# Performance work log

Hardware: AMD Instinct MI355X
Metric: run time of the kernel (lower is better)

Reference implementation:

```python
import jax, jax.numpy as jnp
import numpy as np

B = 8192
D_S, D_W, D_P, D_E, D_C, D_Z = 1024, 1024, 512, 1024, 512, 512
H_P = 2 * D_P          # particle hidden_dim default
RANK = D_W // 4        # low-rank A factor
EPS = 1e-5             # torch LayerNorm default eps


def _ln(x, g, b):
    m = jnp.mean(x, axis=-1, keepdims=True)
    v = jnp.var(x, axis=-1, keepdims=True)
    return (x - m) * jax.lax.rsqrt(v + EPS) * g + b


def setup_inputs() -> dict:
    key = jax.random.key(0)
    ks = iter(jax.random.split(key, 48))
    def randn(shape, scale=1.0):
        return jax.random.normal(next(ks), shape, dtype=jnp.float32) * scale
    def lin(dout, din):  # torch Linear: W [out,in], b [out]
        s = 1.0 / np.sqrt(din)
        return randn((dout, din), s), randn((dout,), s)
    inp = {}
    inp["s_prev"] = randn((B, D_S))
    inp["w_prev"] = randn((B, D_W))
    inp["p_prev"] = randn((B, D_P))
    inp["e_t"] = randn((B, D_E))
    inp["c_t"] = randn((B, D_C))
    d_in = D_S + D_E + D_C
    # fusion_net: Linear -> LN -> ReLU -> Linear
    inp["fw1"], inp["fb1"] = lin(2 * D_Z, d_in)
    inp["fln_g"] = jnp.ones((2 * D_Z,), jnp.float32)
    inp["fln_b"] = jnp.zeros((2 * D_Z,), jnp.float32)
    inp["fw2"], inp["fb2"] = lin(D_Z, 2 * D_Z)
    # wave subsystem
    inp["A_diag"] = jnp.zeros((D_W,), jnp.float32)
    inp["A_U"] = randn((D_W, RANK), 0.01)
    inp["A_V"] = randn((D_W, RANK), 0.01)
    inp["amod_w"], inp["amod_b"] = lin(D_W, D_C)
    inp["bnet_w"], inp["bnet_b"] = lin(D_W, D_C + D_Z)
    # particle subsystem phi
    inp["pw1"], inp["pb1"] = lin(H_P, D_P + D_Z + D_C)
    inp["pln_g"] = jnp.ones((H_P,), jnp.float32)
    inp["pln_b"] = jnp.zeros((H_P,), jnp.float32)
    inp["pw2"], inp["pb2"] = lin(H_P // 2, H_P)
    inp["pw3"], inp["pb3"] = lin(D_P, H_P // 2)
    # gate + mixing projections + output norm
    inp["gw"], inp["gb"] = lin(D_S, d_in)
    inp["uw"] = randn((D_S, D_W), 1.0 / np.sqrt(D_W))
    inp["up"] = randn((D_S, D_P), 1.0 / np.sqrt(D_P))
    inp["oln_g"] = jnp.ones((D_S,), jnp.float32)
    inp["oln_b"] = jnp.zeros((D_S,), jnp.float32)
    return inp


def reference(s_prev, w_prev, p_prev, e_t, c_t,
              fw1, fb1, fln_g, fln_b, fw2, fb2,
              A_diag, A_U, A_V, amod_w, amod_b, bnet_w, bnet_b,
              pw1, pb1, pln_g, pln_b, pw2, pb2, pw3, pb3,
              gw, gb, uw, up, oln_g, oln_b):
    # fusion: z_t = Linear(ReLU(LN(Linear([s||e||c]))))
    fin = jnp.concatenate([s_prev, e_t, c_t], axis=-1)      # [B, d_s+d_e+d_c]
    h = jax.nn.relu(_ln(fin @ fw1.T + fb1, fln_g, fln_b))
    z_t = h @ fw2.T + fb2                                   # [B, d_z]
    # wave: A = (diag(tanh(A_diag)*0.9) + A_U A_V^T) * mod[None,:]
    # so (A w)[b,i] = sum_j A_base[i,j] * (mod*w)[b,j] -> (mod*w) @ A_base^T
    A_base = jnp.diag(jnp.tanh(A_diag) * 0.9) + A_U @ A_V.T  # [d_w, d_w]
    mod = jnp.tanh(c_t @ amod_w.T + amod_b)                  # [B, d_w]
    w_linear = (mod * w_prev) @ A_base.T
    b_in = jnp.concatenate([c_t, z_t], axis=-1)
    w_t = w_linear + b_in @ bnet_w.T + bnet_b                # [B, d_w]
    # particle: p_t = p_prev + tanh(MLP([p||z||c]))
    pin = jnp.concatenate([p_prev, z_t, c_t], axis=-1)
    h1 = jax.nn.relu(_ln(pin @ pw1.T + pb1, pln_g, pln_b))
    h2 = jax.nn.relu(h1 @ pw2.T + pb2)
    p_t = p_prev + jnp.tanh(h2 @ pw3.T + pb3)                # [B, d_p]
    # gated mixing
    g_t = jax.nn.sigmoid(fin @ gw.T + gb)                    # [B, d_s]
    s_t = s_prev + g_t * (p_t @ up.T) + (1.0 - g_t) * (w_t @ uw.T)
    s_t = _ln(s_t, oln_g, oln_b)
    return (s_t, w_t, p_t)
```

## Files before the change

kernel.cpp:

```cpp
#include <hip/hip_runtime.h>
#include <math.h>

typedef unsigned short u16;
typedef __attribute__((ext_vector_type(8))) short short8;
typedef __attribute__((ext_vector_type(4))) float f32x4;

#define AS1C(p) ((const __attribute__((address_space(1))) void*)(p))
#define AS3(p)  ((__attribute__((address_space(3))) void*)(p))

static __device__ __forceinline__ float b2f(u16 h) {
    union { unsigned u; float f; } c; c.u = ((unsigned)h) << 16; return c.f;
}
static __device__ __forceinline__ u16 f2b(float f) {
    union { float f; unsigned u; } c; c.f = f;
    unsigned r = c.u + 0x7FFFu + ((c.u >> 16) & 1u);
    return (u16)(r >> 16);
}

#define EP_NONE     0
#define EP_RELU     1
#define EP_SIGMOID  2
#define EP_TANH_MUL 3
#define EP_TANH_ADD 4
#define EP_DIAG     5

struct GDesc {
    const u16* A;
    const u16* W;
    const float* bias;
    const float* auxf;
    u16* outb;
    float* outf;
    int lda, ldd, N, K, ep, nbm;
};

struct GArgs { GDesc d0, d1, d2; int s1, s2; };

__global__ __launch_bounds__(512, 2)
void gemm_v2(GArgs ga)
{
    __shared__ __align__(16) u16 LDS[65536];

    const int bid = (int)blockIdx.x;
    GDesc dd = (bid < ga.s1) ? ga.d0 : ((bid < ga.s2) ? ga.d1 : ga.d2);
    const int b = bid - ((bid < ga.s1) ? 0 : ((bid < ga.s2) ? ga.s1 : ga.s2));

    const int tid  = threadIdx.x;
    const int lane = tid & 63;
    const int wid  = tid >> 6;
    const int wr   = wid >> 2;
    const int wc   = wid & 3;

    const int bm = b % dd.nbm;
    const int bn = b / dd.nbm;
    const int lda = dd.lda, K = dd.K, N = dd.N, ldd = dd.ldd;
    const int nkt = K >> 6;

    const int srow  = tid >> 3;
    const int sslot = tid & 7;
    const int sgcol = (sslot ^ (srow & 7)) * 8;
    const u16* Ag = dd.A + (size_t)(bm * 256 + srow) * lda + sgcol;
    const u16* Wg = dd.W + (size_t)(bn * 256 + srow) * K + sgcol;
    const int ldst = tid * 8;

    f32x4 acc[8][4];
#pragma unroll
    for (int m = 0; m < 8; ++m)
#pragma unroll
        for (int n = 0; n < 4; ++n) acc[m][n] = (f32x4){0.f, 0.f, 0.f, 0.f};

    const int swz  = (lane & 7) << 4;
    const int cnat = (lane >> 4) << 4;
    const int aRow = (wr * 64 + (lane & 15)) * 64;
    const int bRow = (wc * 32 + (lane & 15)) * 64;
    const u16* pA00 = LDS + aRow + ((cnat ^ swz) >> 1);
    const u16* pA10 = LDS + aRow + ((((64) | cnat) ^ swz) >> 1);
    const u16* pA01 = pA00 + 32768;
    const u16* pA11 = pA10 + 32768;
    const u16* pB00 = LDS + 16384 + bRow + ((cnat ^ swz) >> 1);
    const u16* pB10 = LDS + 16384 + bRow + ((((64) | cnat) ^ swz) >> 1);
    const u16* pB01 = pB00 + 32768;
    const u16* pB11 = pB10 + 32768;

    short8 A0f[4][2], A1f[4][2], B0f[2][2], B1f[2][2];

#define READ_A(AF, PK0, PK1, MHOFF)                                              \
    {                                                                            \
        _Pragma("unroll")                                                        \
        for (int mm = 0; mm < 4; ++mm) {                                         \
            AF[mm][0] = *(const short8*)((PK0) + (MHOFF) + mm * 1024);           \
            AF[mm][1] = *(const short8*)((PK1) + (MHOFF) + mm * 1024);           \
        }                                                                        \
    }
#define READ_B(BF, PK0, PK1, NHOFF)                                              \
    {                                                                            \
        _Pragma("unroll")                                                        \
        for (int nn = 0; nn < 2; ++nn) {                                         \
            BF[nn][0] = *(const short8*)((PK0) + (NHOFF) + nn * 1024);           \
            BF[nn][1] = *(const short8*)((PK1) + (NHOFF) + nn * 1024);           \
        }                                                                        \
    }

#define STAGE_A(bufi, k0_, h)                                                    \
    {                                                                            \
        u16* d_ = &LDS[(bufi) * 32768 + ldst];                                   \
        _Pragma("unroll")                                                        \
        for (int j = 2 * (h); j < 2 * (h) + 2; ++j)                              \
            __builtin_amdgcn_global_load_lds(AS1C(Ag + (size_t)(j * 64) * lda + (k0_)), \
                                             AS3(d_ + j * 4096), 16, 0, 0);      \
    }
#define STAGE_B(bufi, k0_, h)                                                    \
    {                                                                            \
        u16* d_ = &LDS[(bufi) * 32768 + 16384 + ldst];                           \
        _Pragma("unroll")                                                        \
        for (int j = 2 * (h); j < 2 * (h) + 2; ++j)                              \
            __builtin_amdgcn_global_load_lds(AS1C(Wg + (size_t)(j * 64) * K + (k0_)),   \
                                             AS3(d_ + j * 4096), 16, 0, 0);      \
    }

#define VW4()                                                                    \
    {                                                                            \
        __builtin_amdgcn_sched_barrier(0);                                       \
        asm volatile("s_waitcnt vmcnt(4)" ::: "memory");                         \
        __builtin_amdgcn_sched_barrier(0);                                       \
        __builtin_amdgcn_s_barrier();                                            \
        __builtin_amdgcn_sched_barrier(0);                                       \
    }

#define QMFMA(AF, BF, mh, nh)                                                    \
    {                                                                            \
        __builtin_amdgcn_s_setprio(1);                                           \
        _Pragma("unroll")                                                        \
        for (int mm = 0; mm < 4; ++mm)                                           \
            _Pragma("unroll")                                                    \
            for (int nn = 0; nn < 2; ++nn)                                       \
                _Pragma("unroll")                                                \
                for (int ks = 0; ks < 2; ++ks)                                   \
                    acc[(mh) * 4 + mm][(nh) * 2 + nn] =                          \
                        __builtin_amdgcn_mfma_f32_16x16x32_bf16(                 \
                            AF[mm][ks], BF[nn][ks], acc[(mh) * 4 + mm][(nh) * 2 + nn], 0, 0, 0); \
        __builtin_amdgcn_s_setprio(0);                                           \
    }

#define TILE(NBUF, CA0, CA1, CBp0, CBp1, NA0, NA1, NBp0, NBp1, ktv)              \
    {                                                                            \
        const int ka_ = ((ktv) + 1 < nkt) ? (ktv) + 1 : nkt - 1;                 \
        const int k0n = ka_ << 6;                                                \
            \
        STAGE_A(NBUF, k0n, 0);                                                   \
        VW4();                                                                   \
        QMFMA(A0f, B0f, 0, 0);                                                   \
        READ_B(B1f, CBp0, CBp1, 8192);                                           \
            \
        STAGE_B(NBUF, k0n, 0);                                                   \
        VW4();                                                                   \
        QMFMA(A0f, B1f, 0, 1);                                                   \
        READ_A(A1f, CA0, CA1, 8192);                                             \
         \
        STAGE_B(NBUF, k0n, 1);                                                   \
        VW4();                                                                   \
        QMFMA(A1f, B1f, 1, 1);                                                   \
        READ_A(A0f, NA0, NA1, 0);                                                \
         \
        STAGE_A(NBUF, k0n, 1);                                                   \
        VW4();                                                                   \
        QMFMA(A1f, B0f, 1, 0);                                                   \
        READ_B(B0f, NBp0, NBp1, 0);                                              \
    }

    STAGE_A(0, 0, 0);
    __builtin_amdgcn_sched_barrier(0);
    STAGE_B(0, 0, 0);
    __builtin_amdgcn_sched_barrier(0);
    STAGE_B(0, 0, 1);
    __builtin_amdgcn_sched_barrier(0);
    STAGE_A(0, 0, 1);
    __builtin_amdgcn_sched_barrier(0);
    asm volatile("s_waitcnt vmcnt(4)" ::: "memory");
    __builtin_amdgcn_sched_barrier(0);
    __builtin_amdgcn_s_barrier();
    __builtin_amdgcn_sched_barrier(0);
    READ_A(A0f, pA00, pA10, 0);
    READ_B(B0f, pB00, pB10, 0);

    for (int kt = 0; kt < nkt; kt += 2) {
        TILE(1, pA00, pA10, pB00, pB10, pA01, pA11, pB01, pB11, kt);
        TILE(0, pA01, pA11, pB01, pB11, pA00, pA10, pB00, pB10, kt + 1);
    }

#undef READ_A
#undef READ_B
#undef STAGE_A
#undef STAGE_B
#undef VW4
#undef QMFMA
#undef TILE

    const int ep = dd.ep;
#pragma unroll
    for (int n = 0; n < 4; ++n) {
        const int C = bn * 256 + (n >> 1) * 128 + wc * 32 + (n & 1) * 16 + (lane & 15);
        const float bv = dd.bias ? dd.bias[C] : 0.f;
#pragma unroll
        for (int m = 0; m < 8; ++m) {
            const int R0 = bm * 256 + (m >> 2) * 128 + wr * 64 + (m & 3) * 16 + ((lane >> 4) << 2);
#pragma unroll
            for (int j = 0; j < 4; ++j) {
                const int R = R0 + j;
                float v = acc[m][n][j] + bv;
                if (ep == EP_RELU)          v = fmaxf(v, 0.f);
                else if (ep == EP_SIGMOID)  v = 1.f / (1.f + expf(-v));
                else if (ep == EP_TANH_MUL) v = tanhf(v) * dd.auxf[(size_t)R * N + C];
                else if (ep == EP_TANH_ADD) v = dd.auxf[(size_t)R * N + C] + tanhf(v);
                else if (ep == EP_DIAG)     { if (R == C) v += 0.9f * tanhf(dd.auxf[R]); }
                dd.outb[(size_t)R * ldd + C] = f2b(v);
                if (dd.outf) dd.outf[(size_t)R * N + C] = v;
            }
        }
    }
}

template<bool RELU>
__global__ __launch_bounds__(256)
void ln1024(u16* __restrict__ X, const float* __restrict__ gam, const float* __restrict__ bet)
{
    const int row = blockIdx.x;
    u16* xp = X + (size_t)row * 1024 + threadIdx.x * 4;
    u16 loc[4];
    *(uint2*)loc = *(const uint2*)xp;
    float x0 = b2f(loc[0]), x1 = b2f(loc[1]), x2 = b2f(loc[2]), x3 = b2f(loc[3]);
    float s = x0 + x1 + x2 + x3;
    float q = x0 * x0 + x1 * x1 + x2 * x2 + x3 * x3;
#pragma unroll
    for (int off = 32; off; off >>= 1) { s += __shfl_xor(s, off); q += __shfl_xor(q, off); }
    __shared__ float sm[8];
    const int wave = threadIdx.x >> 6, lane = threadIdx.x & 63;
    if (lane == 0) { sm[wave] = s; sm[4 + wave] = q; }
    __syncthreads();
    s = sm[0] + sm[1] + sm[2] + sm[3];
    q = sm[4] + sm[5] + sm[6] + sm[7];
    const float mean = s * (1.f / 1024.f);
    const float var  = q * (1.f / 1024.f) - mean * mean;
    const float inv  = rsqrtf(var + 1e-5f);
    const int cb = threadIdx.x * 4;
#pragma unroll
    for (int j = 0; j < 4; ++j) {
        float y = (b2f(loc[j]) - mean) * inv * gam[cb + j] + bet[cb + j];
        if (RELU) y = fmaxf(y, 0.f);
        loc[j] = f2b(y);
    }
    *(uint2*)xp = *(uint2*)loc;
}

__global__ __launch_bounds__(256)
void mix_ln(const float* __restrict__ sp, const u16* __restrict__ gt,
            const u16* __restrict__ pm, const u16* __restrict__ wm,
            const float* __restrict__ og, const float* __restrict__ ob,
            float* __restrict__ out)
{
    const int row = blockIdx.x;
    const size_t base = (size_t)row * 1024 + threadIdx.x * 4;
    float4 lsp = *(const float4*)(sp + base);
    u16 lg[4], lp[4], lw[4];
    *(uint2*)lg = *(const uint2*)(gt + base);
    *(uint2*)lp = *(const uint2*)(pm + base);
    *(uint2*)lw = *(const uint2*)(wm + base);
    float x[4];
    const float* lspp = (const float*)&lsp;
#pragma unroll
    for (int j = 0; j < 4; ++j) {
        float g = b2f(lg[j]);
        x[j] = lspp[j] + g * b2f(lp[j]) + (1.f - g) * b2f(lw[j]);
    }
    float s = x[0] + x[1] + x[2] + x[3];
    float q = x[0]*x[0] + x[1]*x[1] + x[2]*x[2] + x[3]*x[3];
#pragma unroll
    for (int off = 32; off; off >>= 1) { s += __shfl_xor(s, off); q += __shfl_xor(q, off); }
    __shared__ float sm[8];
    const int wave = threadIdx.x >> 6, lane = threadIdx.x & 63;
    if (lane == 0) { sm[wave] = s; sm[4 + wave] = q; }
    __syncthreads();
    s = sm[0] + sm[1] + sm[2] + sm[3];
    q = sm[4] + sm[5] + sm[6] + sm[7];
    const float mean = s * (1.f / 1024.f);
    const float var  = q * (1.f / 1024.f) - mean * mean;
    const float inv  = rsqrtf(var + 1e-5f);
    const int cb = threadIdx.x * 4;
    float4 o;
    float* op = (float*)&o;
#pragma unroll
    for (int j = 0; j < 4; ++j)
        op[j] = (x[j] - mean) * inv * og[cb + j] + ob[cb + j];
    *(float4*)(out + base) = o;
}

struct CDesc { const void* src; u16* dst; int srcCols8; int dstStride; int dstOff; unsigned end; int isbf16; };
struct CArgs { CDesc d[16]; unsigned total; };

__global__ __launch_bounds__(256)
void multi_copy(CArgs ca)
{
    const unsigned idx = blockIdx.x * 256 + threadIdx.x;
    if (idx >= ca.total) return;
    int i = 0; unsigned start = 0;
    while (idx >= ca.d[i].end) { start = ca.d[i].end; ++i; }
    const CDesc cd = ca.d[i];
    const unsigned local = idx - start;
    const int r = local / cd.srcCols8;
    const int c = local % cd.srcCols8;
    u16 o[8];
    if (cd.isbf16) {
        *(uint4*)o = *(const uint4*)((const u16*)cd.src + ((size_t)r * cd.srcCols8 + c) * 8);
    } else {
        const float* s = (const float*)cd.src + ((size_t)r * cd.srcCols8 + c) * 8;
        const float4 a = *(const float4*)s;
        const float4 bq = *(const float4*)(s + 4);
        const float* ap = (const float*)&a;
        const float* bp = (const float*)&bq;
#pragma unroll
        for (int j = 0; j < 4; ++j) { o[j] = f2b(ap[j]); o[4 + j] = f2b(bp[j]); }
    }
    *(uint4*)(cd.dst + (size_t)r * cd.dstStride + cd.dstOff + (size_t)c * 8) = *(uint4*)o;
}

extern "C" void kernel_launch(void* const* d_in, const int* in_sizes, int n_in,
                              void* d_out, int out_size, void* d_ws, size_t ws_size,
                              hipStream_t stream)
{
    const float* s_prev = (const float*)d_in[0];
    const float* w_prev = (const float*)d_in[1];
    const float* p_prev = (const float*)d_in[2];
    const float* e_t    = (const float*)d_in[3];
    const float* c_t    = (const float*)d_in[4];
    const float* fw1    = (const float*)d_in[5];
    const float* fb1    = (const float*)d_in[6];
    const float* fln_g  = (const float*)d_in[7];
    const float* fln_b  = (const float*)d_in[8];
    const float* fw2    = (const float*)d_in[9];
    const float* fb2    = (const float*)d_in[10];
    const float* A_diag = (const float*)d_in[11];
    const float* A_U    = (const float*)d_in[12];
    const float* A_V    = (const float*)d_in[13];
    const float* amod_w = (const float*)d_in[14];
    const float* amod_b = (const float*)d_in[15];
    const float* bnet_w = (const float*)d_in[16];
    const float* bnet_b = (const float*)d_in[17];
    const float* pw1    = (const float*)d_in[18];
    const float* pb1    = (const float*)d_in[19];
    const float* pln_g  = (const float*)d_in[20];
    const float* pln_b  = (const float*)d_in[21];
    const float* pw2    = (const float*)d_in[22];
    const float* pb2    = (const float*)d_in[23];
    const float* pw3    = (const float*)d_in[24];
    const float* pb3    = (const float*)d_in[25];
    const float* gw     = (const float*)d_in[26];
    const float* gb     = (const float*)d_in[27];
    const float* uw     = (const float*)d_in[28];
    const float* up     = (const float*)d_in[29];
    const float* oln_g  = (const float*)d_in[30];
    const float* oln_b  = (const float*)d_in[31];

    float* out_s = (float*)d_out;
    float* out_w = out_s + (size_t)8192 * 1024;
    float* out_p = out_w + (size_t)8192 * 1024;

    u16* ws = (u16*)d_ws;
    u16* FIN  = ws;
    u16* W_bf = ws + 12582912;
    u16* H    = ws + 20971520;
    u16* P_bf = H;
    u16* Z    = ws + 29360128;
    u16* G    = ws + 33554432;
    u16* ACAT = ws + 41943040;
    u16* PM   = ACAT;
    u16* WM   = ACAT + 8388608;
    u16* WCAT = ws + 58720256;
    u16* wb   = ws + 60817408;
    u16* fw1b  = wb;
    u16* gwb   = wb + 2621440;
    u16* fw2b  = wb + 5242880;
    u16* amodb = wb + 5767168;
    u16* pw1b  = wb + 6291456;
    u16* pw2b  = wb + 7864320;
    u16* pw3b  = wb + 8388608;
    u16* uwb   = wb + 8650752;
    u16* upb   = wb + 9699328;
    u16* AUb   = wb + 10223616;
    u16* AVb   = wb + 10485760;

    const dim3 blk(256);
    const dim3 blk512(512);

    {
        CArgs ca; unsigned cum = 0; int nd = 0;
        auto push = [&](const void* src, u16* dst, int cols8, int stride, int off,
                        int rows, int isbf) {
            cum += (unsigned)rows * cols8;
            ca.d[nd++] = CDesc{src, dst, cols8, stride, off, cum, isbf};
        };
        push(fw1,    fw1b,  320, 2560, 0,    1024, 0);
        push(gw,     gwb,   320, 2560, 0,    1024, 0);
        push(fw2,    fw2b,  128, 1024, 0,    512,  0);
        push(amod_w, amodb, 64,  512,  0,    1024, 0);
        push(pw1,    pw1b,  192, 1536, 0,    1024, 0);
        push(pw2,    pw2b,  128, 1024, 0,    512,  0);
        push(pw3,    pw3b,  64,  512,  0,    512,  0);
        push(uw,     uwb,   128, 1024, 0,    1024, 0);
        push(up,     upb,   64,  512,  0,    1024, 0);
        push(A_U,    AUb,   32,  256,  0,    1024, 0);
        push(A_V,    AVb,   32,  256,  0,    1024, 0);
        push(s_prev, FIN,   128, 2560, 0,    8192, 0);
        push(e_t,    FIN,   128, 2560, 1024, 8192, 0);
        push(c_t,    FIN,   64,  2560, 2048, 8192, 0);
        push(c_t,    ACAT,  64,  2048, 1024, 8192, 0);
        push(bnet_w, WCAT,  128, 2048, 1024, 1024, 0);
        ca.total = cum;
        multi_copy<<<dim3((cum + 255) / 256), blk, 0, stream>>>(ca);
    }

    {
        GArgs ga;
        ga.d0 = GDesc{FIN, fw1b, fb1, nullptr, H, nullptr, 2560, 1024, 1024, 2560, EP_NONE,    32};
        ga.d1 = GDesc{FIN, gwb,  gb,  nullptr, G, nullptr, 2560, 1024, 1024, 2560, EP_SIGMOID, 32};
        ga.d2 = ga.d1; ga.s1 = 128; ga.s2 = 256;
        gemm_v2<<<dim3(256), blk512, 0, stream>>>(ga);
    }
    ln1024<true><<<8192, blk, 0, stream>>>(H, fln_g, fln_b);

    {
        GArgs ga;
        ga.d0 = GDesc{H,          fw2b,  fb2,     nullptr, Z,    nullptr, 1024, 512,  512,  1024, EP_NONE,     32};
        ga.d1 = GDesc{FIN + 2048, amodb, amod_b,  w_prev,  ACAT, nullptr, 2560, 2048, 1024, 512,  EP_TANH_MUL, 32};
        ga.d2 = GDesc{AUb,        AVb,   nullptr, A_diag,  WCAT, nullptr, 256,  2048, 1024, 256,  EP_DIAG,     4};
        ga.s1 = 64; ga.s2 = 192;
        gemm_v2<<<dim3(208), blk512, 0, stream>>>(ga);
    }

    {
        CArgs ca; unsigned cum = 0; int nd = 0;
        auto push = [&](const void* src, u16* dst, int cols8, int stride, int off,
                        int rows, int isbf) {
            cum += (unsigned)rows * cols8;
            ca.d[nd++] = CDesc{src, dst, cols8, stride, off, cum, isbf};
        };
        push(p_prev, FIN,  64, 1536, 0,    8192, 0);
        push(Z,      FIN,  64, 1536, 512,  8192, 1);
        push(c_t,    FIN,  64, 1536, 1024, 8192, 0);
        push(Z,      ACAT, 64, 2048, 1536, 8192, 1);
        ca.total = cum;
        multi_copy<<<dim3((cum + 255) / 256), blk, 0, stream>>>(ca);
    }

    {
        GArgs ga;
        ga.d0 = GDesc{ACAT, WCAT, bnet_b, nullptr, W_bf, out_w,   2048, 1024, 1024, 2048, EP_NONE, 32};
        ga.d1 = GDesc{FIN,  pw1b, pb1,    nullptr, H,    nullptr, 1536, 1024, 1024, 1536, EP_NONE, 32};
        ga.d2 = ga.d1; ga.s1 = 128; ga.s2 = 256;
        gemm_v2<<<dim3(256), blk512, 0, stream>>>(ga);
    }
    ln1024<true><<<8192, blk, 0, stream>>>(H, pln_g, pln_b);

    {
        GArgs ga;
        ga.d0 = GDesc{H,    pw2b, pb2,     nullptr, Z,  nullptr, 1024, 512,  512,  1024, EP_RELU, 32};
        ga.d1 = GDesc{W_bf, uwb,  nullptr, nullptr, WM, nullptr, 1024, 1024, 1024, 1024, EP_NONE, 32};
        ga.d2 = ga.d1; ga.s1 = 64; ga.s2 = 192;
        gemm_v2<<<dim3(192), blk512, 0, stream>>>(ga);
    }

    {
        GArgs ga;
        ga.d0 = GDesc{Z, pw3b, pb3, p_prev, P_bf, out_p, 512, 512, 512, 512, EP_TANH_ADD, 32};
        ga.d1 = ga.d0; ga.d2 = ga.d0; ga.s1 = 64; ga.s2 = 64;
        gemm_v2<<<dim3(64), blk512, 0, stream>>>(ga);
    }

    {
        GArgs ga;
        ga.d0 = GDesc{P_bf, upb, nullptr, nullptr, PM, nullptr, 512, 1024, 1024, 512, EP_NONE, 32};
        ga.d1 = ga.d0; ga.d2 = ga.d0; ga.s1 = 128; ga.s2 = 128;
        gemm_v2<<<dim3(128), blk512, 0, stream>>>(ga);
    }

    mix_ln<<<8192, blk, 0, stream>>>(s_prev, G, PM, WM, oln_g, oln_b, out_s);
}
```

Baseline: 519.3 us.

## Simplify GEMM main loop to whole-tile staging with two barriers per k-tile

Replaces the fine-grained four-phase pipeline, which interleaved partial A/B global-to-LDS stages with vmcnt(4) waits and prefetched fragments for the next tile, with one bulk stage of all A and B loads per k-tile. Each tile is now bracketed by two barriers and the fragments are read at the start of the tile. This cuts barrier count and scheduling complexity, but loses register-level prefetch across tiles and the finer overlap of loads with MFMA work. The vmcnt(8) wait appears to let the current tile's loads finish while the next tile's eight loads stay in flight.

Result: slower. 550.5 us (+6.0%).

```diff
diff --git a/kernel.cpp b/kernel.cpp
--- a/kernel.cpp
+++ b/kernel.cpp
@@ -37,7 +37,7 @@
 struct GArgs { GDesc d0, d1, d2; int s1, s2; };
 
 __global__ __launch_bounds__(512, 2)
-void gemm_v2(GArgs ga)
+void gemm_v3(GArgs ga)
 {
     __shared__ __align__(16) u16 LDS[65536];
 
@@ -101,30 +101,18 @@
         }                                                                        \
     }
 
-#define STAGE_A(bufi, k0_, h)                                                    \
+#define STAGE_ALL(bufi, k0_)                                                     \
     {                                                                            \
-        u16* d_ = &LDS[(bufi) * 32768 + ldst];                                   \
+        u16* al_ = &LDS[(bufi) * 32768 + ldst];                                  \
+        u16* bl_ = &LDS[(bufi) * 32768 + 16384 + ldst];                          \
         _Pragma("unroll")                                                        \
-        for (int j = 2 * (h); j < 2 * (h) + 2; ++j)                              \
+        for (int j = 0; j < 4; ++j)                                              \
             __builtin_amdgcn_global_load_lds(AS1C(Ag + (size_t)(j * 64) * lda + (k0_)), \
-                                             AS3(d_ + j * 4096), 16, 0, 0);      \
-    }
-#define STAGE_B(bufi, k0_, h)                                                    \
-    {                                                                            \
-        u16* d_ = &LDS[(bufi) * 32768 + 16384 + ldst];                           \
+                                             AS3(al_ + j * 4096), 16, 0, 0);     \
         _Pragma("unroll")                                                        \
-        for (int j = 2 * (h); j < 2 * (h) + 2; ++j)                              \
+        for (int j = 0; j < 4; ++j)                                              \
             __builtin_amdgcn_global_load_lds(AS1C(Wg + (size_t)(j * 64) * K + (k0_)),   \
-                                             AS3(d_ + j * 4096), 16, 0, 0);      \
-    }
-
-#define VW4()                                                                    \
-    {                                                                            \
-        __builtin_amdgcn_sched_barrier(0);                                       \
-        asm volatile("s_waitcnt vmcnt(4)" ::: "memory");                         \
-        __builtin_amdgcn_sched_barrier(0);                                       \
-        __builtin_amdgcn_s_barrier();                                            \
-        __builtin_amdgcn_sched_barrier(0);                                       \
+                                             AS3(bl_ + j * 4096), 16, 0, 0);     \
     }
 
 #define QMFMA(AF, BF, mh, nh)                                                    \
@@ -142,57 +130,43 @@
         __builtin_amdgcn_s_setprio(0);                                           \
     }
 
-#define TILE(NBUF, CA0, CA1, CBp0, CBp1, NA0, NA1, NBp0, NBp1, ktv)              \
+#define TILE(NBUF, CA0, CA1, CBp0, CBp1, ktv)                                    \
     {                                                                            \
         const int ka_ = ((ktv) + 1 < nkt) ? (ktv) + 1 : nkt - 1;                 \
         const int k0n = ka_ << 6;                                                \
-            \
-        STAGE_A(NBUF, k0n, 0);                                                   \
-        VW4();                                                                   \
+        __builtin_amdgcn_s_barrier();                \
+        __builtin_amdgcn_sched_barrier(0);                                       \
+        STAGE_ALL(NBUF, k0n);                                                    \
+        __builtin_amdgcn_sched_barrier(0);                                       \
+        asm volatile("s_waitcnt vmcnt(8)" ::: "memory");                         \
+        __builtin_amdgcn_sched_barrier(0);                                       \
+        __builtin_amdgcn_s_barrier();                  \
+        __builtin_amdgcn_sched_barrier(0);                                       \
+        READ_A(A0f, CA0, CA1, 0);                                                \
+        READ_B(B0f, CBp0, CBp1, 0);                                              \
         QMFMA(A0f, B0f, 0, 0);                                                   \
         READ_B(B1f, CBp0, CBp1, 8192);                                           \
-            \
-        STAGE_B(NBUF, k0n, 0);                                                   \
-        VW4();                                                                   \
         QMFMA(A0f, B1f, 0, 1);                                                   \
         READ_A(A1f, CA0, CA1, 8192);                                             \
-         \
-        STAGE_B(NBUF, k0n, 1);                                                   \
-        VW4();                                                                   \
         QMFMA(A1f, B1f, 1, 1);                                                   \
-        READ_A(A0f, NA0, NA1, 0);                                                \
-         \
-        STAGE_A(NBUF, k0n, 1);                                                   \
-        VW4();                                                                   \
         QMFMA(A1f, B0f, 1, 0);                                                   \
-        READ_B(B0f, NBp0, NBp1, 0);                                              \
-    }
-
-    STAGE_A(0, 0, 0);
+    }
+
+    STAGE_ALL(0, 0);
     __builtin_amdgcn_sched_barrier(0);
-    STAGE_B(0, 0, 0);
-    __builtin_amdgcn_sched_barrier(0);
-    STAGE_B(0, 0, 1);
-    __builtin_amdgcn_sched_barrier(0);
-    STAGE_A(0, 0, 1);
-    __builtin_amdgcn_sched_barrier(0);
-    asm volatile("s_waitcnt vmcnt(4)" ::: "memory");
+    asm volatile("s_waitcnt vmcnt(0)" ::: "memory");
     __builtin_amdgcn_sched_barrier(0);
     __builtin_amdgcn_s_barrier();
     __builtin_amdgcn_sched_barrier(0);
-    READ_A(A0f, pA00, pA10, 0);
-    READ_B(B0f, pB00, pB10, 0);
 
     for (int kt = 0; kt < nkt; kt += 2) {
-        TILE(1, pA00, pA10, pB00, pB10, pA01, pA11, pB01, pB11, kt);
-        TILE(0, pA01, pA11, pB01, pB11, pA00, pA10, pB00, pB10, kt + 1);
+        TILE(1, pA00, pA10, pB00, pB10, kt);
+        TILE(0, pA01, pA11, pB01, pB11, kt + 1);
     }
 
 #undef READ_A
 #undef READ_B
-#undef STAGE_A
-#undef STAGE_B
-#undef VW4
+#undef STAGE_ALL
 #undef QMFMA
 #undef TILE
 
@@ -423,7 +397,7 @@
         ga.d0 = GDesc{FIN, fw1b, fb1, nullptr, H, nullptr, 2560, 1024, 1024, 2560, EP_NONE,    32};
         ga.d1 = GDesc{FIN, gwb,  gb,  nullptr, G, nullptr, 2560, 1024, 1024, 2560, EP_SIGMOID, 32};
         ga.d2 = ga.d1; ga.s1 = 128; ga.s2 = 256;
-        gemm_v2<<<dim3(256), blk512, 0, stream>>>(ga);
+        gemm_v3<<<dim3(256), blk512, 0, stream>>>(ga);
     }
     ln1024<true><<<8192, blk, 0, stream>>>(H, fln_g, fln_b);
 
@@ -433,7 +407,7 @@
         ga.d1 = GDesc{FIN + 2048, amodb, amod_b,  w_prev,  ACAT, nullptr, 2560, 2048, 1024, 512,  EP_TANH_MUL, 32};
         ga.d2 = GDesc{AUb,        AVb,   nullptr, A_diag,  WCAT, nullptr, 256,  2048, 1024, 256,  EP_DIAG,     4};
         ga.s1 = 64; ga.s2 = 192;
-        gemm_v2<<<dim3(208), blk512, 0, stream>>>(ga);
+        gemm_v3<<<dim3(208), blk512, 0, stream>>>(ga);
     }
 
     {
@@ -456,7 +430,7 @@
         ga.d0 = GDesc{ACAT, WCAT, bnet_b, nullptr, W_bf, out_w,   2048, 1024, 1024, 2048, EP_NONE, 32};
         ga.d1 = GDesc{FIN,  pw1b, pb1,    nullptr, H,    nullptr, 1536, 1024, 1024, 1536, EP_NONE, 32};
         ga.d2 = ga.d1; ga.s1 = 128; ga.s2 = 256;
-        gemm_v2<<<dim3(256), blk512, 0, stream>>>(ga);
+        gemm_v3<<<dim3(256), blk512, 0, stream>>>(ga);
     }
     ln1024<true><<<8192, blk, 0, stream>>>(H, pln_g, pln_b);
 
@@ -465,21 +439,21 @@
         ga.d0 = GDesc{H,    pw2b, pb2,     nullptr, Z,  nullptr, 1024, 512,  512,  1024, EP_RELU, 32};
         ga.d1 = GDesc{W_bf, uwb,  nullptr, nullptr, WM, nullptr, 1024, 1024, 1024, 1024, EP_NONE, 32};
         ga.d2 = ga.d1; ga.s1 = 64; ga.s2 = 192;
-        gemm_v2<<<dim3(192), blk512, 0, stream>>>(ga);
+        gemm_v3<<<dim3(192), blk512, 0, stream>>>(ga);
     }
 
     {
         GArgs ga;
         ga.d0 = GDesc{Z, pw3b, pb3, p_prev, P_bf, out_p, 512, 512, 512, 512, EP_TANH_ADD, 32};
         ga.d1 = ga.d0; ga.d2 = ga.d0; ga.s1 = 64; ga.s2 = 64;
-        gemm_v2<<<dim3(64), blk512, 0, stream>>>(ga);
+        gemm_v3<<<dim3(64), blk512, 0, stream>>>(ga);
     }
 
     {
         GArgs ga;
         ga.d0 = GDesc{P_bf, upb, nullptr, nullptr, PM, nullptr, 512, 1024, 1024, 512, EP_NONE, 32};
         ga.d1 = ga.d0; ga.d2 = ga.d0; ga.s1 = 128; ga.s2 = 128;
-        gemm_v2<<<dim3(128), blk512, 0, stream>>>(ga);
+        gemm_v3<<<dim3(128), blk512, 0, stream>>>(ga);
     }
 
     mix_ln<<<8192, blk, 0, stream>>>(s_prev, G, PM, WM, oln_g, oln_b, out_s);
```

## Restructure GEMM main loop into deeper prefetch pipeline with split barriers

Applied to the files above, without the earlier changes.

Reorders the GEMM k-loop so that LDS fragment reads happen at the start of each quarter-tile and global-to-LDS staging runs further ahead: one A half is prefetched a full tile in advance, and the wait allows six outstanding loads. A second barrier after each MFMA group is added so that a buffer is not overwritten while other waves may still be reading it. The aim is to hide global load latency more completely. In exchange there are twice as many barriers per tile, and LDS reads sit directly before the MFMAs with an lgkmcnt(0) wait, which may expose LDS latency.

Result: no change. 527.6 us (+1.6%).

```diff
diff --git a/kernel.cpp b/kernel.cpp
--- a/kernel.cpp
+++ b/kernel.cpp
@@ -37,7 +37,7 @@
 struct GArgs { GDesc d0, d1, d2; int s1, s2; };
 
 __global__ __launch_bounds__(512, 2)
-void gemm_v2(GArgs ga)
+void gemm_v4(GArgs ga)
 {
     __shared__ __align__(16) u16 LDS[65536];
 
@@ -118,14 +118,18 @@
                                              AS3(d_ + j * 4096), 16, 0, 0);      \
     }
 
-#define VW4()                                                                    \
-    {                                                                            \
-        __builtin_amdgcn_sched_barrier(0);                                       \
-        asm volatile("s_waitcnt vmcnt(4)" ::: "memory");                         \
-        __builtin_amdgcn_sched_barrier(0);                                       \
-        __builtin_amdgcn_s_barrier();                                            \
-        __builtin_amdgcn_sched_barrier(0);                                       \
-    }
+#define VWB()                                                                    \
+    __builtin_amdgcn_sched_barrier(0);                                           \
+    asm volatile("s_waitcnt vmcnt(6)" ::: "memory");                             \
+    __builtin_amdgcn_sched_barrier(0);                                           \
+    __builtin_amdgcn_s_barrier();                                                \
+    asm volatile("s_waitcnt lgkmcnt(0)" ::: "memory");                           \
+    __builtin_amdgcn_sched_barrier(0);
+
+#define CLB()                                                                    \
+    __builtin_amdgcn_sched_barrier(0);                                           \
+    __builtin_amdgcn_s_barrier();                                                \
+    __builtin_amdgcn_sched_barrier(0);
 
 #define QMFMA(AF, BF, mh, nh)                                                    \
     {                                                                            \
@@ -142,57 +146,63 @@
         __builtin_amdgcn_s_setprio(0);                                           \
     }
 
-#define TILE(NBUF, CA0, CA1, CBp0, CBp1, NA0, NA1, NBp0, NBp1, ktv)              \
-    {                                                                            \
-        const int ka_ = ((ktv) + 1 < nkt) ? (ktv) + 1 : nkt - 1;                 \
-        const int k0n = ka_ << 6;                                                \
-            \
-        STAGE_A(NBUF, k0n, 0);                                                   \
-        VW4();                                                                   \
+#define TILE(CBUF, NBUF, CA0, CA1, CB0, CB1, k0n, k0nn)                          \
+    {                                                                            \
+                                                                   \
+        READ_A(A0f, CA0, CA1, 0);                                                \
+        READ_B(B0f, CB0, CB1, 0);                                                \
+        STAGE_B(NBUF, k0n, 0);                                                   \
+        VWB();                                                                   \
         QMFMA(A0f, B0f, 0, 0);                                                   \
-        READ_B(B1f, CBp0, CBp1, 8192);                                           \
-            \
-        STAGE_B(NBUF, k0n, 0);                                                   \
-        VW4();                                                                   \
+        CLB();                                                                   \
+                                                                   \
+        READ_B(B1f, CB0, CB1, 8192);                                             \
+        STAGE_B(NBUF, k0n, 1);                                                   \
+        VWB();                                                                   \
         QMFMA(A0f, B1f, 0, 1);                                                   \
+        CLB();                                                                   \
+                                                                   \
         READ_A(A1f, CA0, CA1, 8192);                                             \
-         \
-        STAGE_B(NBUF, k0n, 1);                                                   \
-        VW4();                                                                   \
+        STAGE_A(NBUF, k0n, 1);                                                   \
+        VWB();                                                                   \
         QMFMA(A1f, B1f, 1, 1);                                                   \
-        READ_A(A0f, NA0, NA1, 0);                                                \
-         \
-        STAGE_A(NBUF, k0n, 1);                                                   \
-        VW4();                                                                   \
+        CLB();                                                                   \
+                        \
+        STAGE_A(CBUF, k0nn, 0);                                                  \
+        VWB();                                                                   \
         QMFMA(A1f, B0f, 1, 0);                                                   \
-        READ_B(B0f, NBp0, NBp1, 0);                                              \
-    }
-
-    STAGE_A(0, 0, 0);
-    __builtin_amdgcn_sched_barrier(0);
-    STAGE_B(0, 0, 0);
-    __builtin_amdgcn_sched_barrier(0);
-    STAGE_B(0, 0, 1);
-    __builtin_amdgcn_sched_barrier(0);
-    STAGE_A(0, 0, 1);
-    __builtin_amdgcn_sched_barrier(0);
-    asm volatile("s_waitcnt vmcnt(4)" ::: "memory");
-    __builtin_amdgcn_sched_barrier(0);
-    __builtin_amdgcn_s_barrier();
-    __builtin_amdgcn_sched_barrier(0);
-    READ_A(A0f, pA00, pA10, 0);
-    READ_B(B0f, pB00, pB10, 0);
+        CLB();                                                                   \
+    }
+
+    {
+        const int kp1 = ((nkt > 1) ? 1 : 0) << 6;
+        STAGE_A(0, 0, 0);
+        STAGE_B(0, 0, 0);
+        STAGE_B(0, 0, 1);
+        STAGE_A(0, 0, 1);
+        STAGE_A(1, kp1, 0);
+        __builtin_amdgcn_sched_barrier(0);
+        asm volatile("s_waitcnt vmcnt(6)" ::: "memory");
+        __builtin_amdgcn_sched_barrier(0);
+        __builtin_amdgcn_s_barrier();
+        __builtin_amdgcn_sched_barrier(0);
+    }
 
     for (int kt = 0; kt < nkt; kt += 2) {
-        TILE(1, pA00, pA10, pB00, pB10, pA01, pA11, pB01, pB11, kt);
-        TILE(0, pA01, pA11, pB01, pB11, pA00, pA10, pB00, pB10, kt + 1);
+        const int ka1 = ((kt + 1 < nkt) ? kt + 1 : nkt - 1) << 6;
+        const int ka2 = ((kt + 2 < nkt) ? kt + 2 : nkt - 1) << 6;
+        const int kb1 = ka2;
+        const int kb2 = ((kt + 3 < nkt) ? kt + 3 : nkt - 1) << 6;
+        TILE(0, 1, pA00, pA10, pB00, pB10, ka1, ka2);
+        TILE(1, 0, pA01, pA11, pB01, pB11, kb1, kb2);
     }
 
 #undef READ_A
 #undef READ_B
 #undef STAGE_A
 #undef STAGE_B
-#undef VW4
+#undef VWB
+#undef CLB
 #undef QMFMA
 #undef TILE
 
@@ -423,7 +433,7 @@
         ga.d0 = GDesc{FIN, fw1b, fb1, nullptr, H, nullptr, 2560, 1024, 1024, 2560, EP_NONE,    32};
         ga.d1 = GDesc{FIN, gwb,  gb,  nullptr, G, nullptr, 2560, 1024, 1024, 2560, EP_SIGMOID, 32};
         ga.d2 = ga.d1; ga.s1 = 128; ga.s2 = 256;
-        gemm_v2<<<dim3(256), blk512, 0, stream>>>(ga);
+        gemm_v4<<<dim3(256), blk512, 0, stream>>>(ga);
     }
     ln1024<true><<<8192, blk, 0, stream>>>(H, fln_g, fln_b);
 
@@ -433,7 +443,7 @@
         ga.d1 = GDesc{FIN + 2048, amodb, amod_b,  w_prev,  ACAT, nullptr, 2560, 2048, 1024, 512,  EP_TANH_MUL, 32};
         ga.d2 = GDesc{AUb,        AVb,   nullptr, A_diag,  WCAT, nullptr, 256,  2048, 1024, 256,  EP_DIAG,     4};
         ga.s1 = 64; ga.s2 = 192;
-        gemm_v2<<<dim3(208), blk512, 0, stream>>>(ga);
+        gemm_v4<<<dim3(208), blk512, 0, stream>>>(ga);
     }
 
     {
@@ -456,7 +466,7 @@
         ga.d0 = GDesc{ACAT, WCAT, bnet_b, nullptr, W_bf, out_w,   2048, 1024, 1024, 2048, EP_NONE, 32};
         ga.d1 = GDesc{FIN,  pw1b, pb1,    nullptr, H,    nullptr, 1536, 1024, 1024, 1536, EP_NONE, 32};
         ga.d2 = ga.d1; ga.s1 = 128; ga.s2 = 256;
-        gemm_v2<<<dim3(256), blk512, 0, stream>>>(ga);
+        gemm_v4<<<dim3(256), blk512, 0, stream>>>(ga);
     }
     ln1024<true><<<8192, blk, 0, stream>>>(H, pln_g, pln_b);
 
@@ -465,21 +475,21 @@
         ga.d0 = GDesc{H,    pw2b, pb2,     nullptr, Z,  nullptr, 1024, 512,  512,  1024, EP_RELU, 32};
         ga.d1 = GDesc{W_bf, uwb,  nullptr, nullptr, WM, nullptr, 1024, 1024, 1024, 1024, EP_NONE, 32};
         ga.d2 = ga.d1; ga.s1 = 64; ga.s2 = 192;
-        gemm_v2<<<dim3(192), blk512, 0, stream>>>(ga);
+        gemm_v4<<<dim3(192), blk512, 0, stream>>>(ga);
     }
 
     {
         GArgs ga;
         ga.d0 = GDesc{Z, pw3b, pb3, p_prev, P_bf, out_p, 512, 512, 512, 512, EP_TANH_ADD, 32};
         ga.d1 = ga.d0; ga.d2 = ga.d0; ga.s1 = 64; ga.s2 = 64;
-        gemm_v2<<<dim3(64), blk512, 0, stream>>>(ga);
+        gemm_v4<<<dim3(64), blk512, 0, stream>>>(ga);
     }
 
     {
         GArgs ga;
         ga.d0 = GDesc{P_bf, upb, nullptr, nullptr, PM, nullptr, 512, 1024, 1024, 512, EP_NONE, 32};
         ga.d1 = ga.d0; ga.d2 = ga.d0; ga.s1 = 128; ga.s2 = 128;
-        gemm_v2<<<dim3(128), blk512, 0, stream>>>(ga);
+        gemm_v4<<<dim3(128), blk512, 0, stream>>>(ga);
     }
 
     mix_ln<<<8192, blk, 0, stream>>>(s_prev, G, PM, WM, oln_g, oln_b, out_s);
```

## Add 128x128 GEMM kernel for small launches and fuse Z copy into epilogue

Applied to the files above, without the earlier changes.

Adds a smaller-tile GEMM (128x128, 256 threads, single-buffered) and uses it for the launches that previously ran only 64 to 208 large-tile blocks (fw2/amod/A_base, pw3, up). These launches now spread across many more blocks to fill the GPU's compute units. The fw2 epilogue also writes Z directly into the ACAT buffer through a second output pointer, which removes one segment of the copy kernel. The cost is a simpler, non-pipelined inner loop with less data reuse per block.

New measurement: 496.1 us. 4.5% less time.

```diff
diff --git a/kernel.cpp b/kernel.cpp
--- a/kernel.cpp
+++ b/kernel.cpp
@@ -31,7 +31,8 @@
     const float* auxf;
     u16* outb;
     float* outf;
-    int lda, ldd, N, K, ep, nbm;
+    u16* outb2;
+    int lda, ldd, N, K, ep, nbm, ldd2, coff2;
 };
 
 struct GArgs { GDesc d0, d1, d2; int s1, s2; };
@@ -146,22 +147,18 @@
     {                                                                            \
         const int ka_ = ((ktv) + 1 < nkt) ? (ktv) + 1 : nkt - 1;                 \
         const int k0n = ka_ << 6;                                                \
-            \
         STAGE_A(NBUF, k0n, 0);                                                   \
         VW4();                                                                   \
         QMFMA(A0f, B0f, 0, 0);                                                   \
         READ_B(B1f, CBp0, CBp1, 8192);                                           \
-            \
         STAGE_B(NBUF, k0n, 0);                                                   \
         VW4();                                                                   \
         QMFMA(A0f, B1f, 0, 1);                                                   \
         READ_A(A1f, CA0, CA1, 8192);                                             \
-         \
         STAGE_B(NBUF, k0n, 1);                                                   \
         VW4();                                                                   \
         QMFMA(A1f, B1f, 1, 1);                                                   \
         READ_A(A0f, NA0, NA1, 0);                                                \
-         \
         STAGE_A(NBUF, k0n, 1);                                                   \
         VW4();                                                                   \
         QMFMA(A1f, B0f, 1, 0);                                                   \
@@ -215,6 +212,106 @@
                 else if (ep == EP_DIAG)     { if (R == C) v += 0.9f * tanhf(dd.auxf[R]); }
                 dd.outb[(size_t)R * ldd + C] = f2b(v);
                 if (dd.outf) dd.outf[(size_t)R * N + C] = v;
+            }
+        }
+    }
+}
+
+__global__ __launch_bounds__(256)
+void gemm_s(GArgs ga)
+{
+    __shared__ __align__(16) u16 As[8192];
+    __shared__ __align__(16) u16 Bs[8192];
+
+    const int bid = (int)blockIdx.x;
+    GDesc dd = (bid < ga.s1) ? ga.d0 : ((bid < ga.s2) ? ga.d1 : ga.d2);
+    const int b = bid - ((bid < ga.s1) ? 0 : ((bid < ga.s2) ? ga.s1 : ga.s2));
+
+    const int tid  = threadIdx.x;
+    const int lane = tid & 63;
+    const int wave = tid >> 6;
+    const int wr   = wave >> 1;
+    const int wc   = wave & 1;
+
+    const int bm = b % dd.nbm;
+    const int bn = b / dd.nbm;
+    const int lda = dd.lda, K = dd.K, N = dd.N, ldd = dd.ldd;
+
+    const int srow  = tid >> 3;
+    const int sslot = tid & 7;
+    const int sgcol = (sslot ^ (srow & 7)) * 8;
+    const u16* Ab = dd.A + (size_t)(bm * 128 + srow) * lda + sgcol;
+    const u16* Wb = dd.W + (size_t)(bn * 128 + srow) * K + sgcol;
+    u16* Asl = As + srow * 64 + sslot * 8;
+    u16* Bsl = Bs + srow * 64 + sslot * 8;
+
+    f32x4 acc[4][4];
+#pragma unroll
+    for (int m = 0; m < 4; ++m)
+#pragma unroll
+        for (int n = 0; n < 4; ++n) acc[m][n] = (f32x4){0.f, 0.f, 0.f, 0.f};
+
+    const int swz  = (lane & 7) << 4;
+    const int cnat = (lane >> 4) << 4;
+    const u16* pa0 = As + ((wr * 64) + (lane & 15)) * 64 + ((cnat ^ swz) >> 1);
+    const u16* pa1 = As + ((wr * 64) + (lane & 15)) * 64 + ((((64) | cnat) ^ swz) >> 1);
+    const u16* pb0 = Bs + ((wc * 64) + (lane & 15)) * 64 + ((cnat ^ swz) >> 1);
+    const u16* pb1 = Bs + ((wc * 64) + (lane & 15)) * 64 + ((((64) | cnat) ^ swz) >> 1);
+
+    for (int k0 = 0; k0 < K; k0 += 64) {
+#pragma unroll
+        for (int i = 0; i < 4; ++i) {
+            __builtin_amdgcn_global_load_lds(AS1C(Ab + (size_t)(i * 32) * lda + k0),
+                                             AS3(Asl + i * 32 * 64), 16, 0, 0);
+            __builtin_amdgcn_global_load_lds(AS1C(Wb + (size_t)(i * 32) * K + k0),
+                                             AS3(Bsl + i * 32 * 64), 16, 0, 0);
+        }
+        __syncthreads();
+        short8 a[4][2], bb[4][2];
+#pragma unroll
+        for (int m = 0; m < 4; ++m) {
+            a[m][0] = *(const short8*)(pa0 + m * 1024);
+            a[m][1] = *(const short8*)(pa1 + m * 1024);
+        }
+#pragma unroll
+        for (int n = 0; n < 4; ++n) {
+            bb[n][0] = *(const short8*)(pb0 + n * 1024);
+            bb[n][1] = *(const short8*)(pb1 + n * 1024);
+        }
+#pragma unroll
+        for (int m = 0; m < 4; ++m)
+#pragma unroll
+            for (int n = 0; n < 4; ++n)
+#pragma unroll
+                for (int ks = 0; ks < 2; ++ks)
+                    acc[m][n] = __builtin_amdgcn_mfma_f32_16x16x32_bf16(
+                        a[m][ks], bb[n][ks], acc[m][n], 0, 0, 0);
+        __syncthreads();
+    }
+
+    const int rbase = bm * 128 + wr * 64 + ((lane >> 4) << 2);
+    const int cbase = bn * 128 + wc * 64 + (lane & 15);
+    const int ep = dd.ep;
+#pragma unroll
+    for (int n = 0; n < 4; ++n) {
+        const int C = cbase + n * 16;
+        const float bv = dd.bias ? dd.bias[C] : 0.f;
+#pragma unroll
+        for (int m = 0; m < 4; ++m) {
+            const int R0 = rbase + m * 16;
+#pragma unroll
+            for (int j = 0; j < 4; ++j) {
+                const int R = R0 + j;
+                float v = acc[m][n][j] + bv;
+                if (ep == EP_RELU)          v = fmaxf(v, 0.f);
+                else if (ep == EP_SIGMOID)  v = 1.f / (1.f + expf(-v));
+                else if (ep == EP_TANH_MUL) v = tanhf(v) * dd.auxf[(size_t)R * N + C];
+                else if (ep == EP_TANH_ADD) v = dd.auxf[(size_t)R * N + C] + tanhf(v);
+                else if (ep == EP_DIAG)     { if (R == C) v += 0.9f * tanhf(dd.auxf[R]); }
+                const u16 hb = f2b(v);
+                dd.outb[(size_t)R * ldd + C] = hb;
+                if (dd.outf)  dd.outf[(size_t)R * N + C] = v;
+                if (dd.outb2) dd.outb2[(size_t)R * dd.ldd2 + C + dd.coff2] = hb;
             }
         }
     }
@@ -420,8 +517,8 @@
 
     {
         GArgs ga;
-        ga.d0 = GDesc{FIN, fw1b, fb1, nullptr, H, nullptr, 2560, 1024, 1024, 2560, EP_NONE,    32};
-        ga.d1 = GDesc{FIN, gwb,  gb,  nullptr, G, nullptr, 2560, 1024, 1024, 2560, EP_SIGMOID, 32};
+        ga.d0 = GDesc{FIN, fw1b, fb1, nullptr, H, nullptr, nullptr, 2560, 1024, 1024, 2560, EP_NONE,    32, 0, 0};
+        ga.d1 = GDesc{FIN, gwb,  gb,  nullptr, G, nullptr, nullptr, 2560, 1024, 1024, 2560, EP_SIGMOID, 32, 0, 0};
         ga.d2 = ga.d1; ga.s1 = 128; ga.s2 = 256;
         gemm_v2<<<dim3(256), blk512, 0, stream>>>(ga);
     }
@@ -429,11 +526,11 @@
 
     {
         GArgs ga;
-        ga.d0 = GDesc{H,          fw2b,  fb2,     nullptr, Z,    nullptr, 1024, 512,  512,  1024, EP_NONE,     32};
-        ga.d1 = GDesc{FIN + 2048, amodb, amod_b,  w_prev,  ACAT, nullptr, 2560, 2048, 1024, 512,  EP_TANH_MUL, 32};
-        ga.d2 = GDesc{AUb,        AVb,   nullptr, A_diag,  WCAT, nullptr, 256,  2048, 1024, 256,  EP_DIAG,     4};
-        ga.s1 = 64; ga.s2 = 192;
-        gemm_v2<<<dim3(208), blk512, 0, stream>>>(ga);
+        ga.d0 = GDesc{H,          fw2b,  fb2,     nullptr, Z,    nullptr, ACAT,    1024, 512,  512,  1024, EP_NONE,     64, 2048, 1536};
+        ga.d1 = GDesc{FIN + 2048, amodb, amod_b,  w_prev,  ACAT, nullptr, nullptr, 2560, 2048, 1024, 512,  EP_TANH_MUL, 64, 0, 0};
+        ga.d2 = GDesc{AUb,        AVb,   nullptr, A_diag,  WCAT, nullptr, nullptr, 256,  2048, 1024, 256,  EP_DIAG,     8, 0, 0};
+        ga.s1 = 256; ga.s2 = 768;
+        gemm_s<<<dim3(832), blk, 0, stream>>>(ga);
     }
 
     {
@@ -446,15 +543,14 @@
         push(p_prev, FIN,  64, 1536, 0,    8192, 0);
         push(Z,      FIN,  64, 1536, 512,  8192, 1);
         push(c_t,    FIN,  64, 1536, 1024, 8192, 0);
-        push(Z,      ACAT, 64, 2048, 1536, 8192, 1);
         ca.total = cum;
         multi_copy<<<dim3((cum + 255) / 256), blk, 0, stream>>>(ca);
     }
 
     {
         GArgs ga;
-        ga.d0 = GDesc{ACAT, WCAT, bnet_b, nullptr, W_bf, out_w,   2048, 1024, 1024, 2048, EP_NONE, 32};
-        ga.d1 = GDesc{FIN,  pw1b, pb1,    nullptr, H,    nullptr, 1536, 1024, 1024, 1536, EP_NONE, 32};
+        ga.d0 = GDesc{ACAT, WCAT, bnet_b, nullptr, W_bf, out_w,   nullptr, 2048, 1024, 1024, 2048, EP_NONE, 32, 0, 0};
+        ga.d1 = GDesc{FIN,  pw1b, pb1,    nullptr, H,    nullptr, nullptr, 1536, 1024, 1024, 1536, EP_NONE, 32, 0, 0};
         ga.d2 = ga.d1; ga.s1 = 128; ga.s2 = 256;
         gemm_v2<<<dim3(256), blk512, 0, stream>>>(ga);
     }
@@ -462,24 +558,24 @@
 
     {
         GArgs ga;
-        ga.d0 = GDesc{H,    pw2b, pb2,     nullptr, Z,  nullptr, 1024, 512,  512,  1024, EP_RELU, 32};
-        ga.d1 = GDesc{W_bf, uwb,  nullptr, nullptr, WM, nullptr, 1024, 1024, 1024, 1024, EP_NONE, 32};
+        ga.d0 = GDesc{H,    pw2b, pb2,     nullptr, Z,  nullptr, nullptr, 1024, 512,  512,  1024, EP_RELU, 32, 0, 0};
+        ga.d1 = GDesc{W_bf, uwb,  nullptr, nullptr, WM, nullptr, nullptr, 1024, 1024, 1024, 1024, EP_NONE, 32, 0, 0};
         ga.d2 = ga.d1; ga.s1 = 64; ga.s2 = 192;
         gemm_v2<<<dim3(192), blk512, 0, stream>>>(ga);
     }
 
     {
         GArgs ga;
-        ga.d0 = GDesc{Z, pw3b, pb3, p_prev, P_bf, out_p, 512, 512, 512, 512, EP_TANH_ADD, 32};
-        ga.d1 = ga.d0; ga.d2 = ga.d0; ga.s1 = 64; ga.s2 = 64;
-        gemm_v2<<<dim3(64), blk512, 0, stream>>>(ga);
+        ga.d0 = GDesc{Z, pw3b, pb3, p_prev, P_bf, out_p, nullptr, 512, 512, 512, 512, EP_TANH_ADD, 64, 0, 0};
+        ga.d1 = ga.d0; ga.d2 = ga.d0; ga.s1 = 256; ga.s2 = 256;
+        gemm_s<<<dim3(256), blk, 0, stream>>>(ga);
     }
 
     {
         GArgs ga;
-        ga.d0 = GDesc{P_bf, upb, nullptr, nullptr, PM, nullptr, 512, 1024, 1024, 512, EP_NONE, 32};
-        ga.d1 = ga.d0; ga.d2 = ga.d0; ga.s1 = 128; ga.s2 = 128;
-        gemm_v2<<<dim3(128), blk512, 0, stream>>>(ga);
+        ga.d0 = GDesc{P_bf, upb, nullptr, nullptr, PM, nullptr, nullptr, 512, 1024, 1024, 512, EP_NONE, 64, 0, 0};
+        ga.d1 = ga.d0; ga.d2 = ga.d0; ga.s1 = 512; ga.s2 = 512;
+        gemm_s<<<dim3(512), blk, 0, stream>>>(ga);
     }
 
     mix_ln<<<8192, blk, 0, stream>>>(s_prev, G, PM, WM, oln_g, oln_b, out_s);
```
